# Kernel tuning notes

Measured on AMD Instinct MI355X. Metric: run time of the kernel, lower is better.

## Reference

```python
import jax, jax.numpy as jnp
import numpy as np

EMBED_DIM = 1024
NUM_HEADS = 16
HEAD_DIM = EMBED_DIM // NUM_HEADS
SEQ_LEN = 4096


def setup_inputs() -> dict:
    key = jax.random.key(0)
    kx, kq, kk, kv = jax.random.split(key, 4)
    x = jax.random.normal(kx, (SEQ_LEN, EMBED_DIM), dtype=jnp.float32)
    Wq = jax.random.normal(kq, (EMBED_DIM, EMBED_DIM), dtype=jnp.float32)
    Wk = jax.random.normal(kk, (EMBED_DIM, EMBED_DIM), dtype=jnp.float32)
    Wv = jax.random.normal(kv, (EMBED_DIM, EMBED_DIM), dtype=jnp.float32)
    return {"x": x, "Wq": Wq, "Wk": Wk, "Wv": Wv}


def reference(x, Wq, Wk, Wv):
    seq_len, embed_dim = x.shape
    h, d = NUM_HEADS, HEAD_DIM
    # project then split heads: [S, E] -> [H, S, D]
    q = (x @ Wq).reshape(seq_len, h, d).transpose(1, 0, 2)
    k = (x @ Wk).reshape(seq_len, h, d).transpose(1, 0, 2)
    v = (x @ Wv).reshape(seq_len, h, d).transpose(1, 0, 2)
    # full [H, S, S] scores, scaled by sqrt(head_dim) (faithful to original)
    scores = jnp.einsum("hsd,htd->hst", q, k) / jnp.sqrt(jnp.asarray(d, dtype=q.dtype))
    weights = jax.nn.softmax(scores, axis=-1)
    out = jnp.einsum("hst,htd->hsd", weights, v)  # [H, S, D]
    return out.transpose(1, 0, 2).reshape(seq_len, embed_dim)
```

## Files before the change

kernel.cpp:

```cpp
#include <hip/hip_runtime.h>
#include <hip/hip_bf16.h>

#define SEQ 4096
#define EMB 1024
#define NHD 16
#define HDD 64

using bf16 = __hip_bfloat16;
using bf16x8 = __attribute__((ext_vector_type(8))) short;
using f32x4  = __attribute__((ext_vector_type(4))) float;
using f32x16 = __attribute__((ext_vector_type(16))) float;
using u32x4  = __attribute__((ext_vector_type(4))) unsigned int;
using u32x2  = __attribute__((ext_vector_type(2))) unsigned int;

#define MFMA16(a, b, c) __builtin_amdgcn_mfma_f32_16x16x32_bf16((a), (b), (c), 0, 0, 0)
#define MFMA32(a, b, c) __builtin_amdgcn_mfma_f32_32x32x16_bf16((a), (b), (c), 0, 0, 0)

#define QSCALE 0.1803368801111204f

__device__ __forceinline__ float b2f(bf16 b) { return __bfloat162float(b); }

__device__ __forceinline__ void gll16(const void* g, void* l) {
    __builtin_amdgcn_global_load_lds(
        (const __attribute__((address_space(1))) unsigned int*)g,
        (__attribute__((address_space(3))) unsigned int*)l, 16, 0, 0);
}

__device__ __forceinline__ unsigned pack_bf16x2(float a, float b) {
    __hip_bfloat162 p = __float22bfloat162_rn(make_float2(a, b));
    unsigned w;
    __builtin_memcpy(&w, &p, 4);
    return w;
}

__global__ void split_kernel(const float* __restrict__ src, bf16* __restrict__ hi,
                             bf16* __restrict__ lo, int n4) {
    int i = blockIdx.x * blockDim.x + threadIdx.x;
    if (i >= n4) return;
    float4 v = ((const float4*)src)[i];
    float vv[4] = {v.x, v.y, v.z, v.w};
#pragma unroll
    for (int j = 0; j < 4; j++) {
        bf16 h = __float2bfloat16(vv[j]);
        hi[i * 4 + j] = h;
        lo[i * 4 + j] = __float2bfloat16(vv[j] - b2f(h));
    }
}

__global__ void wtrans_kernel(const float* __restrict__ Wq, const float* __restrict__ Wk,
                              const float* __restrict__ Wv,
                              bf16* __restrict__ thq, bf16* __restrict__ tlq,
                              bf16* __restrict__ thk, bf16* __restrict__ tlk,
                              bf16* __restrict__ thv, bf16* __restrict__ tlv) {
    __shared__ float tile[32][33];
    const float* W;
    bf16 *wth, *wtl;
    if (blockIdx.z == 0) { W = Wq; wth = thq; wtl = tlq; }
    else if (blockIdx.z == 1) { W = Wk; wth = thk; wtl = tlk; }
    else { W = Wv; wth = thv; wtl = tlv; }
    int n0 = blockIdx.x * 32, k0 = blockIdx.y * 32;
    int tx = threadIdx.x, ty = threadIdx.y;
    for (int r = ty; r < 32; r += 8)
        tile[r][tx] = W[(k0 + r) * EMB + n0 + tx];
    __syncthreads();
    for (int r = ty; r < 32; r += 8) {
        float v = tile[tx][r];
        bf16 h = __float2bfloat16(v);
        wth[(n0 + r) * EMB + k0 + tx] = h;
        wtl[(n0 + r) * EMB + k0 + tx] = __float2bfloat16(v - b2f(h));
    }
}

template <int NTERMS>
__device__ __forceinline__ void proj_loop(
    const bf16* __restrict__ Ah, const bf16* __restrict__ Al,
    const bf16* __restrict__ Bth, const bf16* __restrict__ Btl,
    bf16* lAh, bf16* lAl, bf16* lBh, bf16* lBl,
    int m0, int n0, int t, f32x4 (&acc)[4][4]) {
    const int wid = t >> 6, lane = t & 63, lr = lane & 15, lg = lane >> 4;
    const int wr = (wid >> 1) * 64, wc = (wid & 1) * 64;
    for (int k0 = 0; k0 < EMB; k0 += 32) {
#pragma unroll
        for (int c = t; c < 512; c += 256) {
            int row = c >> 2, slot = c & 3;
            *(uint4*)&lAh[row * 40 + slot * 8] =
                *(const uint4*)&Ah[(m0 + row) * EMB + k0 + slot * 8];
            *(uint4*)&lBh[row * 40 + slot * 8] =
                *(const uint4*)&Bth[(n0 + row) * EMB + k0 + slot * 8];
            if constexpr (NTERMS == 3) {
                *(uint4*)&lAl[row * 40 + slot * 8] =
                    *(const uint4*)&Al[(m0 + row) * EMB + k0 + slot * 8];
                *(uint4*)&lBl[row * 40 + slot * 8] =
                    *(const uint4*)&Btl[(n0 + row) * EMB + k0 + slot * 8];
            }
        }
        __syncthreads();
        bf16x8 fah[4], fbh[4], fal[4], fbl[4];
#pragma unroll
        for (int i = 0; i < 4; i++) {
            fah[i] = *(const bf16x8*)&lAh[(wr + i * 16 + lr) * 40 + lg * 8];
            fbh[i] = *(const bf16x8*)&lBh[(wc + i * 16 + lr) * 40 + lg * 8];
            if constexpr (NTERMS == 3) {
                fal[i] = *(const bf16x8*)&lAl[(wr + i * 16 + lr) * 40 + lg * 8];
                fbl[i] = *(const bf16x8*)&lBl[(wc + i * 16 + lr) * 40 + lg * 8];
            }
        }
#pragma unroll
        for (int i = 0; i < 4; i++)
#pragma unroll
            for (int j = 0; j < 4; j++) {
                acc[i][j] = MFMA16(fah[i], fbh[j], acc[i][j]);
                if constexpr (NTERMS == 3) {
                    acc[i][j] = MFMA16(fah[i], fbl[j], acc[i][j]);
                    acc[i][j] = MFMA16(fal[i], fbh[j], acc[i][j]);
                }
            }
        __syncthreads();
    }
}

__global__ __launch_bounds__(256) void proj_qkv(
    const bf16* __restrict__ xh, const bf16* __restrict__ xl,
    const bf16* __restrict__ thq, const bf16* __restrict__ tlq,
    const bf16* __restrict__ thk, const bf16* __restrict__ tlk,
    const bf16* __restrict__ thv,
    bf16* __restrict__ qh, bf16* __restrict__ ql,
    bf16* __restrict__ kh, bf16* __restrict__ kl, bf16* __restrict__ vt) {
    __shared__ __align__(16) bf16 lAh[128 * 40];
    __shared__ __align__(16) bf16 lAl[128 * 40];
    __shared__ __align__(16) bf16 lBh[128 * 40];
    __shared__ __align__(16) bf16 lBl[128 * 40];
    const int t = threadIdx.x;
    const int m0 = blockIdx.y * 128;
    const int which = blockIdx.x >> 3;
    const int n0 = (blockIdx.x & 7) * 128;

    f32x4 acc[4][4];
#pragma unroll
    for (int i = 0; i < 4; i++)
#pragma unroll
        for (int j = 0; j < 4; j++) acc[i][j] = (f32x4){0.f, 0.f, 0.f, 0.f};

    if (which == 0)
        proj_loop<3>(xh, xl, thq, tlq, lAh, lAl, lBh, lBl, m0, n0, t, acc);
    else if (which == 1)
        proj_loop<3>(xh, xl, thk, tlk, lAh, lAl, lBh, lBl, m0, n0, t, acc);
    else
        proj_loop<1>(xh, xl, thv, nullptr, lAh, lAl, lBh, lBl, m0, n0, t, acc);

    const int wid = t >> 6, lane = t & 63, lr = lane & 15, lg = lane >> 4;
    const int wr = (wid >> 1) * 64, wc = (wid & 1) * 64;

    if (which == 2) {
#pragma unroll
        for (int i = 0; i < 4; i++)
#pragma unroll
            for (int j = 0; j < 4; j++) {
                int n = n0 + wc + j * 16 + lr;
                int m = m0 + wr + i * 16 + lg * 4;
                uint2 w;
                w.x = pack_bf16x2(acc[i][j][0], acc[i][j][1]);
                w.y = pack_bf16x2(acc[i][j][2], acc[i][j][3]);
                *(uint2*)&vt[(size_t)n * SEQ + m] = w;
            }
    } else {
        float scale = (which == 0) ? QSCALE : 1.0f;
        bf16* Chi = (which == 0) ? qh : kh;
        bf16* Clo = (which == 0) ? ql : kl;
#pragma unroll
        for (int i = 0; i < 4; i++)
#pragma unroll
            for (int j = 0; j < 4; j++)
#pragma unroll
                for (int q = 0; q < 4; q++) {
                    float cv = acc[i][j][q] * scale;
                    int m = m0 + wr + i * 16 + lg * 4 + q;
                    int n = n0 + wc + j * 16 + lr;
                    bf16 hv = __float2bfloat16(cv);
                    Chi[m * EMB + n] = hv;
                    Clo[m * EMB + n] = __float2bfloat16(cv - b2f(hv));
                }
    }
}

__global__ __launch_bounds__(512, 2) void attn_kernel(
    const bf16* __restrict__ qh, const bf16* __restrict__ ql,
    const bf16* __restrict__ kh, const bf16* __restrict__ kl,
    const bf16* __restrict__ vt, float* __restrict__ out) {
    __shared__ __align__(16) bf16 lKV[2][3][64 * 64];
    const int t = threadIdx.x;
    const int swz = (blockIdx.x & 7) * 32 + (blockIdx.x >> 3);
    const int h = swz >> 4;
    const int q0 = (swz & 15) * 256;
    const int wid = t >> 6, lane = t & 63;
    const int qq = lane & 31, hi = lane >> 5;
    const int qrow = q0 + wid * 32 + qq;

    bf16x8 fqh[4], fql[4];
    {
        const bf16* qbh = qh + (size_t)qrow * EMB + h * HDD + hi * 8;
        const bf16* qbl = ql + (size_t)qrow * EMB + h * HDD + hi * 8;
#pragma unroll
        for (int ds = 0; ds < 4; ds++) {
            fqh[ds] = *(const bf16x8*)(qbh + ds * 16);
            fql[ds] = *(const bf16x8*)(qbl + ds * 16);
        }
    }

    const int srow = lane >> 3, slot = lane & 7;
    const int r = wid * 8 + srow;
    const int sb = (slot ^ (r & 7)) * 16;
    const char* gp[3];
    gp[0] = (const char*)kh + ((size_t)r * EMB + h * HDD) * 2 + sb;
    gp[1] = (const char*)kl + ((size_t)r * EMB + h * HDD) * 2 + sb;
    gp[2] = (const char*)vt + ((size_t)(h * HDD + r) * SEQ) * 2 + sb;
    bf16* lp[3];
#pragma unroll
    for (int i = 0; i < 3; i++) lp[i] = &lKV[0][i][wid * 512];

    f32x16 Ofr[2];
#pragma unroll
    for (int db = 0; db < 2; db++)
#pragma unroll
        for (int rg = 0; rg < 16; rg++) Ofr[db][rg] = 0.f;
    float Mr = -1e30f, Lr = 0.f;

#pragma unroll
    for (int i = 0; i < 3; i++) {
        gll16(gp[i], lp[i]);
        gp[i] += (i < 2) ? (size_t)(64 * EMB * 2) : (size_t)(64 * 2);
    }
    __syncthreads();

    for (int tk = 0; tk < SEQ / 64; tk++) {
        const int cur = tk & 1;
        if (tk < SEQ / 64 - 1) {
#pragma unroll
            for (int i = 0; i < 3; i++) {
                gll16(gp[i], lp[i] + (cur ^ 1) * 12288);
                gp[i] += (i < 2) ? (size_t)(64 * EMB * 2) : (size_t)(64 * 2);
            }
        }
        const char* cKh = (const char*)&lKV[cur][0][0];
        const char* cKl = (const char*)&lKV[cur][1][0];
        const char* cV  = (const char*)&lKV[cur][2][0];

        __builtin_amdgcn_s_setprio(1);
        f32x16 sfr[2];
#pragma unroll
        for (int kb = 0; kb < 2; kb++) {
            const int row = kb * 32 + qq;
            const char* rbh = cKh + row * 128;
            const char* rbl = cKl + row * 128;
            const int sw = (row & 7) << 4;
            f32x16 a;
#pragma unroll
            for (int rg = 0; rg < 16; rg++) a[rg] = 0.f;
#pragma unroll
            for (int ds = 0; ds < 4; ds++) {
                const int off = (ds * 32 + hi * 16) ^ sw;
                bf16x8 kbh_ = *(const bf16x8*)(rbh + off);
                bf16x8 kbl_ = *(const bf16x8*)(rbl + off);
                a = MFMA32(kbh_, fqh[ds], a);
                a = MFMA32(kbh_, fql[ds], a);
                a = MFMA32(kbl_, fqh[ds], a);
            }
            sfr[kb] = a;
        }
        __builtin_amdgcn_s_setprio(0);

        float mx = sfr[0][0];
#pragma unroll
        for (int kb = 0; kb < 2; kb++)
#pragma unroll
            for (int rg = 0; rg < 16; rg++) mx = fmaxf(mx, sfr[kb][rg]);
        mx = fmaxf(mx, __shfl_xor(mx, 32));

        bool resc = !__all(mx <= Mr + 11.5f);
        float mn = resc ? fmaxf(Mr, mx) : Mr;
        float ps = 0.f;
#pragma unroll
        for (int kb = 0; kb < 2; kb++)
#pragma unroll
            for (int rg = 0; rg < 16; rg++) {
                float p = __builtin_exp2f(sfr[kb][rg] - mn);
                sfr[kb][rg] = p;
                ps += p;
            }
        ps += __shfl_xor(ps, 32);
        if (resc) {
            float fac = __builtin_exp2f(Mr - mn);
            Mr = mn;
            Lr = Lr * fac + ps;
#pragma unroll
            for (int db = 0; db < 2; db++)
#pragma unroll
                for (int rg = 0; rg < 16; rg++) Ofr[db][rg] *= fac;
        } else {
            Lr += ps;
        }

        bf16x8 pf[4];
#pragma unroll
        for (int sl = 0; sl < 4; sl++) {
            const int kb = sl >> 1, s8 = (sl & 1) * 8;
            unsigned w01 = pack_bf16x2(sfr[kb][s8 + 0], sfr[kb][s8 + 1]);
            unsigned w23 = pack_bf16x2(sfr[kb][s8 + 2], sfr[kb][s8 + 3]);
            unsigned w45 = pack_bf16x2(sfr[kb][s8 + 4], sfr[kb][s8 + 5]);
            unsigned w67 = pack_bf16x2(sfr[kb][s8 + 6], sfr[kb][s8 + 7]);
            u32x2 r0 = __builtin_amdgcn_permlane32_swap(w01, w45, false, false);
            u32x2 r1 = __builtin_amdgcn_permlane32_swap(w23, w67, false, false);
            u32x4 fw = {r0[0], r1[0], r0[1], r1[1]};
            bf16x8 pfv;
            __builtin_memcpy(&pfv, &fw, 16);
            pf[sl] = pfv;
        }

        __builtin_amdgcn_s_setprio(1);
#pragma unroll
        for (int sl = 0; sl < 4; sl++) {
#pragma unroll
            for (int db = 0; db < 2; db++) {
                const int vd = db * 32 + qq;
                const char* pv =
                    cV + vd * 128 + ((sl * 32 + hi * 16) ^ ((vd & 7) << 4));
                bf16x8 vf = *(const bf16x8*)pv;
                Ofr[db] = MFMA32(vf, pf[sl], Ofr[db]);
            }
        }
        __builtin_amdgcn_s_setprio(0);

        __syncthreads();
    }

    float inv = 1.0f / Lr;
    float* orow = out + (size_t)qrow * EMB + h * HDD;
#pragma unroll
    for (int db = 0; db < 2; db++)
#pragma unroll
        for (int rg = 0; rg < 4; rg++) {
            float4 o = make_float4(Ofr[db][rg * 4 + 0] * inv,
                                   Ofr[db][rg * 4 + 1] * inv,
                                   Ofr[db][rg * 4 + 2] * inv,
                                   Ofr[db][rg * 4 + 3] * inv);
            *(float4*)(orow + db * 32 + rg * 8 + hi * 4) = o;
        }
}

extern "C" void kernel_launch(void* const* d_in, const int* in_sizes, int n_in,
                              void* d_out, int out_size, void* d_ws, size_t ws_size,
                              hipStream_t stream) {
    const float* x = (const float*)d_in[0];
    const float* Wq = (const float*)d_in[1];
    const float* Wk = (const float*)d_in[2];
    const float* Wv = (const float*)d_in[3];
    float* out = (float*)d_out;

    char* ws = (char*)d_ws;
    size_t off = 0;
    auto alloc = [&](size_t elems) -> bf16* {
        bf16* p = (bf16*)(ws + off);
        off += elems * sizeof(bf16);
        return p;
    };
    bf16* xh = alloc((size_t)SEQ * EMB);
    bf16* xl = alloc((size_t)SEQ * EMB);
    bf16* wthq = alloc((size_t)EMB * EMB);
    bf16* wtlq = alloc((size_t)EMB * EMB);
    bf16* wthk = alloc((size_t)EMB * EMB);
    bf16* wtlk = alloc((size_t)EMB * EMB);
    bf16* wthv = alloc((size_t)EMB * EMB);
    bf16* wtlv = alloc((size_t)EMB * EMB);
    bf16* qh = alloc((size_t)SEQ * EMB);
    bf16* ql = alloc((size_t)SEQ * EMB);
    bf16* kh = alloc((size_t)SEQ * EMB);
    bf16* kl = alloc((size_t)SEQ * EMB);
    bf16* vt = alloc((size_t)SEQ * EMB);
    (void)ws_size; (void)in_sizes; (void)n_in; (void)out_size;

    split_kernel<<<(SEQ * EMB / 4 + 255) / 256, 256, 0, stream>>>(x, xh, xl, SEQ * EMB / 4);
    wtrans_kernel<<<dim3(32, 32, 3), dim3(32, 8), 0, stream>>>(
        Wq, Wk, Wv, wthq, wtlq, wthk, wtlk, wthv, wtlv);
    proj_qkv<<<dim3(24, 32), 256, 0, stream>>>(
        xh, xl, wthq, wtlq, wthk, wtlk, wthv, qh, ql, kh, kl, vt);
    attn_kernel<<<256, 512, 0, stream>>>(qh, ql, kh, kl, vt, out);
}
```

Before: 243.4 us.

## Software-pipeline QK^T of next tile with softmax and PV of previous tile

The attention loop is restructured so each iteration computes QK^T scores for key tile t while running the softmax and PV MFMAs on tile t-1's scores. K stays double-buffered in LDS, while V moves to a triple buffer so the V tile for the lagging PV step is not overwritten. The max and sum reductions become balanced trees, and the first MFMA takes a zero vector instead of a zeroed accumulator. The aim is to hide softmax latency behind matrix-core work, at the cost of a second set of live score registers and more LDS, which could cause spills or lower occupancy under the 512x2 launch bound.

```diff
diff --git a/kernel.cpp b/kernel.cpp
--- a/kernel.cpp
+++ b/kernel.cpp
@@ -187,7 +187,8 @@
     const bf16* __restrict__ qh, const bf16* __restrict__ ql,
     const bf16* __restrict__ kh, const bf16* __restrict__ kl,
     const bf16* __restrict__ vt, float* __restrict__ out) {
-    __shared__ __align__(16) bf16 lKV[2][3][64 * 64];
+    __shared__ __align__(16) bf16 lK[2][2][64 * 64];
+    __shared__ __align__(16) bf16 lV[3][64 * 64];
     const int t = threadIdx.x;
     const int swz = (blockIdx.x & 7) * 32 + (blockIdx.x >> 3);
     const int h = swz >> 4;
@@ -210,14 +211,14 @@
     const int srow = lane >> 3, slot = lane & 7;
     const int r = wid * 8 + srow;
     const int sb = (slot ^ (r & 7)) * 16;
-    const char* gp[3];
-    gp[0] = (const char*)kh + ((size_t)r * EMB + h * HDD) * 2 + sb;
-    gp[1] = (const char*)kl + ((size_t)r * EMB + h * HDD) * 2 + sb;
-    gp[2] = (const char*)vt + ((size_t)(h * HDD + r) * SEQ) * 2 + sb;
-    bf16* lp[3];
-#pragma unroll
-    for (int i = 0; i < 3; i++) lp[i] = &lKV[0][i][wid * 512];
-
+    const char* gKh = (const char*)kh + ((size_t)r * EMB + h * HDD) * 2 + sb;
+    const char* gKl = (const char*)kl + ((size_t)r * EMB + h * HDD) * 2 + sb;
+    const char* gV  = (const char*)vt + ((size_t)(h * HDD + r) * SEQ) * 2 + sb;
+    const size_t KSTEP = (size_t)64 * EMB * 2, VSTEP = 64 * 2;
+
+    f32x16 z16;
+#pragma unroll
+    for (int rg = 0; rg < 16; rg++) z16[rg] = 0.f;
     f32x16 Ofr[2];
 #pragma unroll
     for (int db = 0; db < 2; db++)
@@ -225,28 +226,12 @@
         for (int rg = 0; rg < 16; rg++) Ofr[db][rg] = 0.f;
     float Mr = -1e30f, Lr = 0.f;
 
-#pragma unroll
-    for (int i = 0; i < 3; i++) {
-        gll16(gp[i], lp[i]);
-        gp[i] += (i < 2) ? (size_t)(64 * EMB * 2) : (size_t)(64 * 2);
-    }
-    __syncthreads();
-
-    for (int tk = 0; tk < SEQ / 64; tk++) {
-        const int cur = tk & 1;
-        if (tk < SEQ / 64 - 1) {
-#pragma unroll
-            for (int i = 0; i < 3; i++) {
-                gll16(gp[i], lp[i] + (cur ^ 1) * 12288);
-                gp[i] += (i < 2) ? (size_t)(64 * EMB * 2) : (size_t)(64 * 2);
-            }
-        }
-        const char* cKh = (const char*)&lKV[cur][0][0];
-        const char* cKl = (const char*)&lKV[cur][1][0];
-        const char* cV  = (const char*)&lKV[cur][2][0];
-
+    f32x16 sA[2], sB[2];
+
+    auto qkt = [&](int cur, f32x16 (&sOut)[2]) {
+        const char* cKh = (const char*)&lK[cur][0][0];
+        const char* cKl = (const char*)&lK[cur][1][0];
         __builtin_amdgcn_s_setprio(1);
-        f32x16 sfr[2];
 #pragma unroll
         for (int kb = 0; kb < 2; kb++) {
             const int row = kb * 32 + qq;
@@ -255,38 +240,46 @@
             const int sw = (row & 7) << 4;
             f32x16 a;
 #pragma unroll
-            for (int rg = 0; rg < 16; rg++) a[rg] = 0.f;
-#pragma unroll
             for (int ds = 0; ds < 4; ds++) {
                 const int off = (ds * 32 + hi * 16) ^ sw;
                 bf16x8 kbh_ = *(const bf16x8*)(rbh + off);
                 bf16x8 kbl_ = *(const bf16x8*)(rbl + off);
-                a = MFMA32(kbh_, fqh[ds], a);
+                if (ds == 0)
+                    a = MFMA32(kbh_, fqh[0], z16);
+                else
+                    a = MFMA32(kbh_, fqh[ds], a);
                 a = MFMA32(kbh_, fql[ds], a);
                 a = MFMA32(kbl_, fqh[ds], a);
             }
-            sfr[kb] = a;
+            sOut[kb] = a;
         }
         __builtin_amdgcn_s_setprio(0);
-
-        float mx = sfr[0][0];
-#pragma unroll
-        for (int kb = 0; kb < 2; kb++)
-#pragma unroll
-            for (int rg = 0; rg < 16; rg++) mx = fmaxf(mx, sfr[kb][rg]);
+    };
+
+    auto finish = [&](f32x16 (&sIn)[2], const char* cV) {
+        float m8[8];
+#pragma unroll
+        for (int i = 0; i < 8; i++)
+            m8[i] = fmaxf(fmaxf(sIn[0][i], sIn[0][i + 8]),
+                          fmaxf(sIn[1][i], sIn[1][i + 8]));
+        float mx = fmaxf(fmaxf(fmaxf(m8[0], m8[1]), fmaxf(m8[2], m8[3])),
+                         fmaxf(fmaxf(m8[4], m8[5]), fmaxf(m8[6], m8[7])));
         mx = fmaxf(mx, __shfl_xor(mx, 32));
-
         bool resc = !__all(mx <= Mr + 11.5f);
         float mn = resc ? fmaxf(Mr, mx) : Mr;
-        float ps = 0.f;
 #pragma unroll
         for (int kb = 0; kb < 2; kb++)
 #pragma unroll
-            for (int rg = 0; rg < 16; rg++) {
-                float p = __builtin_exp2f(sfr[kb][rg] - mn);
-                sfr[kb][rg] = p;
-                ps += p;
-            }
+            for (int rg = 0; rg < 16; rg++)
+                sIn[kb][rg] = __builtin_exp2f(sIn[kb][rg] - mn);
+        float s16[16];
+#pragma unroll
+        for (int i = 0; i < 16; i++) s16[i] = sIn[0][i] + sIn[1][i];
+        float s8[8];
+#pragma unroll
+        for (int i = 0; i < 8; i++) s8[i] = s16[i] + s16[i + 8];
+        float ps = ((s8[0] + s8[1]) + (s8[2] + s8[3])) +
+                   ((s8[4] + s8[5]) + (s8[6] + s8[7]));
         ps += __shfl_xor(ps, 32);
         if (resc) {
             float fac = __builtin_exp2f(Mr - mn);
@@ -299,15 +292,14 @@
         } else {
             Lr += ps;
         }
-
         bf16x8 pf[4];
 #pragma unroll
         for (int sl = 0; sl < 4; sl++) {
-            const int kb = sl >> 1, s8 = (sl & 1) * 8;
-            unsigned w01 = pack_bf16x2(sfr[kb][s8 + 0], sfr[kb][s8 + 1]);
-            unsigned w23 = pack_bf16x2(sfr[kb][s8 + 2], sfr[kb][s8 + 3]);
-            unsigned w45 = pack_bf16x2(sfr[kb][s8 + 4], sfr[kb][s8 + 5]);
-            unsigned w67 = pack_bf16x2(sfr[kb][s8 + 6], sfr[kb][s8 + 7]);
+            const int kb = sl >> 1, s8i = (sl & 1) * 8;
+            unsigned w01 = pack_bf16x2(sIn[kb][s8i + 0], sIn[kb][s8i + 1]);
+            unsigned w23 = pack_bf16x2(sIn[kb][s8i + 2], sIn[kb][s8i + 3]);
+            unsigned w45 = pack_bf16x2(sIn[kb][s8i + 4], sIn[kb][s8i + 5]);
+            unsigned w67 = pack_bf16x2(sIn[kb][s8i + 6], sIn[kb][s8i + 7]);
             u32x2 r0 = __builtin_amdgcn_permlane32_swap(w01, w45, false, false);
             u32x2 r1 = __builtin_amdgcn_permlane32_swap(w23, w67, false, false);
             u32x4 fw = {r0[0], r1[0], r0[1], r1[1]};
@@ -315,7 +307,6 @@
             __builtin_memcpy(&pfv, &fw, 16);
             pf[sl] = pfv;
         }
-
         __builtin_amdgcn_s_setprio(1);
 #pragma unroll
         for (int sl = 0; sl < 4; sl++) {
@@ -329,9 +320,37 @@
             }
         }
         __builtin_amdgcn_s_setprio(0);
-
+    };
+
+    gll16(gKh, &lK[0][0][wid * 512]); gKh += KSTEP;
+    gll16(gKl, &lK[0][1][wid * 512]); gKl += KSTEP;
+    gll16(gV, &lV[0][wid * 512]);     gV += VSTEP;
+    __syncthreads();
+    gll16(gKh, &lK[1][0][wid * 512]); gKh += KSTEP;
+    gll16(gKl, &lK[1][1][wid * 512]); gKl += KSTEP;
+    gll16(gV, &lV[1][wid * 512]);     gV += VSTEP;
+    qkt(0, sA);
+    __syncthreads();
+
+    auto window = [&](int tt, f32x16 (&sIn)[2], f32x16 (&sOut)[2]) {
+        const int cur = tt & 1;
+        if (tt < 63) {
+            const int vnxt = (tt + 1) % 3;
+            gll16(gKh, &lK[cur ^ 1][0][wid * 512]); gKh += KSTEP;
+            gll16(gKl, &lK[cur ^ 1][1][wid * 512]); gKl += KSTEP;
+            gll16(gV, &lV[vnxt][wid * 512]);        gV += VSTEP;
+        }
+        qkt(cur, sOut);
+        finish(sIn, (const char*)&lV[(tt - 1) % 3][0]);
         __syncthreads();
-    }
+    };
+
+    for (int tt = 1; tt < 63; tt += 2) {
+        window(tt, sA, sB);
+        window(tt + 1, sB, sA);
+    }
+    window(63, sA, sB);
+    finish(sB, (const char*)&lV[63 % 3][0]);
 
     float inv = 1.0f / Lr;
     float* orow = out + (size_t)qrow * EMB + h * HDD;
```

After: 259.0 us. 6.4% more time.
